# Kernel tuning notes

Measured on AMD Instinct MI355X. Metric: run time of the kernel, lower is better.

## Reference

```python
import jax, jax.numpy as jnp
import numpy as np

B, K, R, H = 64, 256, 4, 32


def setup_inputs() -> dict:
    key = jax.random.key(0)
    ks = jax.random.split(key, 24)
    rn = lambda k, s: jax.random.normal(k, s, dtype=jnp.float32)
    # F.normalize(dim=0) on per-sample [n, R] factors -> normalize columns (axis=1 batched)
    norm_cols = lambda x: x / jnp.linalg.norm(x, axis=1, keepdims=True)
    I = jnp.eye(K, dtype=jnp.float32)
    return dict(
        tensor_input=rn(ks[0], (B, 6, K, K)),
        seed_ic=rn(ks[1], (B, K)),
        seed_sir=rn(ks[2], (B, K)),
        seed_ic_conv=rn(ks[3], (B, K)),
        seed_sir_conv=rn(ks[4], (B, K)),
        scalars=rn(ks[5], (B, 2)),
        second_eig_interlink_out=rn(ks[6], (B,)),
        second_eig_interlink_in=rn(ks[7], (B,)),
        S1=I + 0.1 * rn(ks[8], (K, K)),
        S2=I + 0.1 * rn(ks[9], (K, K)),
        S3=I + 0.1 * rn(ks[10], (K, K)),
        S4=I + 0.1 * rn(ks[11], (K, K)),
        # CP factors (fresh random per sample in torch; fixed here for determinism)
        cp_A=norm_cols(rn(ks[12], (B, 6, R))),
        cp_B=norm_cols(rn(ks[13], (B, K, R))),
        cp_C=norm_cols(rn(ks[14], (B, K, R))),
        cp_W1=0.1 * rn(ks[15], (R, H, 3)), cp_b1=jnp.zeros((R, H), jnp.float32),
        cp_w2=0.1 * rn(ks[16], (R, H)), cp_b2=jnp.zeros((R,), jnp.float32),
        seed_W1=0.1 * rn(ks[17], (4, H, K)), seed_b1=jnp.zeros((4, H), jnp.float32),
        seed_w2=0.1 * rn(ks[18], (4, H)), seed_b2=jnp.zeros((4,), jnp.float32),
        fin_W1=0.1 * rn(ks[19], (H, R + 6)), fin_b1=jnp.zeros((H,), jnp.float32),
        fin_w2=0.1 * rn(ks[20], (H,)), fin_b2=jnp.zeros((), jnp.float32),
    )


def reference(tensor_input, seed_ic, seed_sir, seed_ic_conv, seed_sir_conv, scalars,
              second_eig_interlink_out, second_eig_interlink_in,
              S1, S2, S3, S4, cp_A, cp_B, cp_C,
              cp_W1, cp_b1, cp_w2, cp_b2,
              seed_W1, seed_b1, seed_w2, seed_b2,
              fin_W1, fin_b1, fin_w2, fin_b2):
    Kd = S1.shape[0]
    I = jnp.eye(Kd, dtype=tensor_input.dtype)
    ic1, ic2, sir1, sir2 = tensor_input[:, 0], tensor_input[:, 1], tensor_input[:, 2], tensor_input[:, 3]
    Z1r, Z2r = tensor_input[:, 4], tensor_input[:, 5]

    # MatrixTransform chains == plain batched matmuls (custom backward = standard matmul vjp)
    Z1 = ((ic1 @ S1) @ Z1r @ S2) @ jnp.swapaxes(sir2, -1, -2)   # [B,K,K]
    Z2 = ((sir1 @ S3) @ Z2r @ S4) @ jnp.swapaxes(ic2, -1, -2)   # [B,K,K]

    def spec_loss(val, M):
        ev = jnp.linalg.eigvalsh(M)                 # ascending, lower-triangle (matches torch)
        eig_loss = jnp.mean(jnp.abs(val - ev[1:5])) # k = min(5, K) = 5
        diff = jnp.mean(jnp.abs(M - I))             # reg_loss and diff_from_identity are identical
        off_loss = -jnp.mean(jnp.abs(M - jnp.diag(jnp.diag(M))))
        loss = eig_loss + 0.1 * diff + 0.1 * diff + 0.1 * off_loss
        return jnp.where(val != 0.0, loss, jnp.zeros_like(loss))  # torch: `if value`

    spec_out = jax.vmap(spec_loss)(second_eig_interlink_out, Z1).mean()
    spec_in = jax.vmap(spec_loss)(second_eig_interlink_in, Z2).mean()

    # S-matrix regularizers (batch-independent) + per-sample transform loss.
    # The torch list interleaves them, so the mean = 0.5*s_total + 0.5*mean(transform).
    sreg = lambda S: -jnp.mean(jnp.abs(S - I)) - jnp.mean(jnp.abs(S - jnp.diag(jnp.diag(S))))
    s_total = sreg(S1) + sreg(S2) + sreg(S3) + sreg(S4)
    transform = jnp.mean(jnp.abs(Z1 - Z1r), axis=(1, 2)) + jnp.mean(jnp.abs(Z2 - Z2r), axis=(1, 2))
    s_matrix_mean = 0.5 * s_total + 0.5 * transform.mean()

    # CP reconstruction loss on tensor with slots 4,5 replaced by Z1,Z2
    T_upd = jnp.concatenate([tensor_input[:, :4], Z1[:, None], Z2[:, None]], axis=1)  # [B,6,K,K]
    recon = jnp.einsum('bir,bjr,bkr->bijk', cp_A, cp_B, cp_C)
    cp_loss = jnp.mean((recon - T_upd) ** 2)

    # Per-rank tiny MLPs on factor means
    triple = jnp.stack([cp_A.mean(axis=1), cp_B.mean(axis=1), cp_C.mean(axis=1)], axis=-1)  # [B,R,3]
    h = jax.nn.relu(jnp.einsum('brd,rhd->brh', triple, cp_W1) + cp_b1[None])
    cp_s = jnp.einsum('brh,rh->br', h, cp_w2) + cp_b2[None]                                 # [B,R]

    seeds = jnp.stack([seed_ic, seed_sir, seed_ic_conv, seed_sir_conv], axis=1)             # [B,4,K]
    h2 = jax.nn.relu(jnp.einsum('bjk,jhk->bjh', seeds, seed_W1) + seed_b1[None])
    seed_s = jnp.einsum('bjh,jh->bj', h2, seed_w2) + seed_b2[None]                          # [B,4]

    combined = jnp.concatenate([cp_s, seed_s, scalars], axis=1)                             # [B,R+6]
    logits = jax.nn.relu(combined @ fin_W1.T + fin_b1) @ fin_w2 + fin_b2                    # [B]

    return (logits, spec_out, spec_in, cp_loss, s_matrix_mean)
```

## Files before the change

### kernel.cpp

```cpp
#include <hip/hip_runtime.h>
#include <hip/hip_fp16.h>

#define LM 20

#define OFF_MP    0ull
#define OFF_Q0    16777216ull
#define OFF_Q1    33554432ull
#define OFF_ZB    33554432ull
#define OFF_EIG   50331648ull
#define OFF_DIFFP (OFF_EIG + 4096ull)
#define OFF_OFFP  (OFF_DIFFP + 1024ull)
#define OFF_TRP   (OFF_OFFP + 1024ull)
#define OFF_SMALL (OFF_TRP + 1024ull)

typedef unsigned short ushort_t;
typedef short bf16x8 __attribute__((ext_vector_type(8)));
typedef float f32x4 __attribute__((ext_vector_type(4)));

static __device__ __forceinline__ ushort_t f2bf(float f) {
  unsigned u = __float_as_uint(f);
  unsigned r = (u + 0x7fffu + ((u >> 16) & 1u)) >> 16;
  return (ushort_t)r;
}
static __device__ __forceinline__ unsigned packbf(float a, float b) {
  return (unsigned)f2bf(a) | ((unsigned)f2bf(b) << 16);
}
static __device__ __forceinline__ float bflo(unsigned u) { return __uint_as_float(u << 16); }
static __device__ __forceinline__ float bfhi(unsigned u) { return __uint_as_float(u & 0xffff0000u); }
static __device__ __forceinline__ float b2f(ushort_t u) { return __uint_as_float(((unsigned)u) << 16); }
static __device__ __forceinline__ __half2 u2h2(unsigned u) { __half2 r; *reinterpret_cast<unsigned*>(&r) = u; return r; }
static __device__ __forceinline__ unsigned packh2(float a, float b) {
  return (unsigned)__half_as_ushort(__float2half_rn(a)) |
         ((unsigned)__half_as_ushort(__float2half_rn(b)) << 16);
}

template<bool ABF, int BMODE, bool INITP, bool REDUCE>
__global__ __launch_bounds__(256) void gemm_mfma(
    const void* __restrict__ A0, const void* __restrict__ A1, size_t sA,
    const void* __restrict__ B0, const void* __restrict__ B1, size_t sB,
    void* __restrict__ Cbase, size_t sC,
    const float* __restrict__ Zr0, const float* __restrict__ Zr1, size_t sZr,
    double* __restrict__ smallp, double* __restrict__ diffP,
    double* __restrict__ offP, double* __restrict__ trP)
{
  __shared__ ushort_t At[128][40];
  __shared__ ushort_t Bt[128][40];
  __shared__ float redsh[4][3];
  const int t = threadIdx.x;
  if (INITP && blockIdx.x == 0 && blockIdx.y == 0 && blockIdx.z == 0) {
    if (t < 2) smallp[t] = 0.0;
    if (t < 128) { diffP[t] = 0.0; offP[t] = 0.0; trP[t] = 0.0; }
  }
  const int b = blockIdx.z;
  const int bl = (b < 64) ? b : b - 64;
  const void* Ab_ = (b < 64) ? A0 : A1;
  const void* Bb_ = (b < 64) ? B0 : B1;
  const int tm = blockIdx.y * 128, tn = blockIdx.x * 128;
  const int w = t >> 6, l = t & 63;
  const int wr = w >> 1, wc = w & 1;
  const int fr = l & 15, kc = l >> 4;

  f32x4 acc[4][4] = {};

  for (int s8 = 0; s8 < 8; ++s8) {
    const int k0 = s8 << 5;
    #pragma unroll
    for (int cc = 0; cc < 2; ++cc) {
      int c = t + cc * 256;
      int row = c >> 2, q = c & 3;
      if (ABF) {
        const ushort_t* Ap = (const ushort_t*)Ab_ + (size_t)bl * sA + (size_t)(tm + row) * 256 + k0 + q * 8;
        *(uint4*)&At[row][q * 8] = *(const uint4*)Ap;
      } else {
        const float* Ap = (const float*)Ab_ + (size_t)bl * sA + (size_t)(tm + row) * 256 + k0 + q * 8;
        float4 f0 = *(const float4*)Ap, f1 = *(const float4*)(Ap + 4);
        uint4 u;
        u.x = packbf(f0.x, f0.y); u.y = packbf(f0.z, f0.w);
        u.z = packbf(f1.x, f1.y); u.w = packbf(f1.z, f1.w);
        *(uint4*)&At[row][q * 8] = u;
      }
    }
    if (BMODE == 1) {
      #pragma unroll
      for (int cc = 0; cc < 2; ++cc) {
        int c = t + cc * 256;
        int row = c >> 2, q = c & 3;
        const float* Bp = (const float*)Bb_ + (size_t)bl * sB + (size_t)(tn + row) * 256 + k0 + q * 8;
        float4 f0 = *(const float4*)Bp, f1 = *(const float4*)(Bp + 4);
        uint4 u;
        u.x = packbf(f0.x, f0.y); u.y = packbf(f0.z, f0.w);
        u.z = packbf(f1.x, f1.y); u.w = packbf(f1.z, f1.w);
        *(uint4*)&Bt[row][q * 8] = u;
      }
    } else {
      int k2 = t & 15, c = t >> 4;
      const float* Bp0 = (const float*)Bb_ + (size_t)bl * sB + (size_t)(k0 + 2 * k2) * 256 + tn + c * 8;
      const float* Bp1 = Bp0 + 256;
      float4 a0 = *(const float4*)Bp0, a1 = *(const float4*)(Bp0 + 4);
      float4 c0v = *(const float4*)Bp1, c1v = *(const float4*)(Bp1 + 4);
      float lo[8] = {a0.x,a0.y,a0.z,a0.w,a1.x,a1.y,a1.z,a1.w};
      float hi[8] = {c0v.x,c0v.y,c0v.z,c0v.w,c1v.x,c1v.y,c1v.z,c1v.w};
      unsigned* Bd = (unsigned*)&Bt[0][0];
      #pragma unroll
      for (int i = 0; i < 8; ++i) {
        int n = c * 8 + i;
        Bd[n * 20 + k2] = packbf(lo[i], hi[i]);
      }
    }
    __syncthreads();
    bf16x8 af[4], bfv[4];
    #pragma unroll
    for (int i = 0; i < 4; ++i) af[i] = *(const bf16x8*)&At[wr * 64 + i * 16 + fr][kc * 8];
    #pragma unroll
    for (int jj = 0; jj < 4; ++jj) bfv[jj] = *(const bf16x8*)&Bt[wc * 64 + jj * 16 + fr][kc * 8];
    #pragma unroll
    for (int i = 0; i < 4; ++i) {
      #pragma unroll
      for (int jj = 0; jj < 4; ++jj) {
        acc[i][jj] = __builtin_amdgcn_mfma_f32_16x16x32_bf16(af[i], bfv[jj], acc[i][jj], 0, 0, 0);
      }
    }
    __syncthreads();
  }

  ushort_t* Cp = (ushort_t*)Cbase + (size_t)b * sC;
  #pragma unroll
  for (int i = 0; i < 4; ++i) {
    #pragma unroll
    for (int q = 0; q < 4; ++q) {
      size_t rbase = (size_t)(tm + wr * 64 + i * 16 + kc * 4 + q) * 256;
      #pragma unroll
      for (int jj = 0; jj < 4; ++jj) {
        Cp[rbase + tn + wc * 64 + jj * 16 + fr] = f2bf(acc[i][jj][q]);
      }
    }
  }

  if (REDUCE) {
    const float* Zr_ = ((b < 64) ? Zr0 : Zr1) + (size_t)bl * sZr;
    float pd = 0.f, po = 0.f, ptr = 0.f;
    #pragma unroll
    for (int i = 0; i < 4; ++i) {
      #pragma unroll
      for (int q = 0; q < 4; ++q) {
        int row = tm + wr * 64 + i * 16 + kc * 4 + q;
        const float* ZrRow = Zr_ + (size_t)row * 256 + tn + wc * 64;
        #pragma unroll
        for (int jj = 0; jj < 4; ++jj) {
          int col = tn + wc * 64 + jj * 16 + fr;
          float c = acc[i][jj][q];
          float zr = ZrRow[jj * 16 + fr];
          bool diag = (row == col);
          pd += fabsf(c - (diag ? 1.0f : 0.0f));
          po += diag ? 0.0f : fabsf(c);
          ptr += fabsf(c - zr);
        }
      }
    }
    #pragma unroll
    for (int off = 32; off > 0; off >>= 1) {
      pd += __shfl_down(pd, off);
      po += __shfl_down(po, off);
      ptr += __shfl_down(ptr, off);
    }
    if (l == 0) { redsh[w][0] = pd; redsh[w][1] = po; redsh[w][2] = ptr; }
    __syncthreads();
    if (t == 0) {
      atomicAdd(&diffP[b], (double)(redsh[0][0] + redsh[1][0] + redsh[2][0] + redsh[3][0]));
      atomicAdd(&offP[b],  (double)(redsh[0][1] + redsh[1][1] + redsh[2][1] + redsh[3][1]));
      atomicAdd(&trP[b],   (double)(redsh[0][2] + redsh[1][2] + redsh[2][2] + redsh[3][2]));
    }
  }
}

__global__ __launch_bounds__(256) void symm_t(const ushort_t* __restrict__ Zb,
                                              unsigned* __restrict__ Mp)
{
  __shared__ unsigned Au[64][38];
  __shared__ unsigned Bu[64][38];
  const int blk = blockIdx.x;
  const int mtx = blk / 10, p = blk - mtx * 10;
  const int bi_t[10] = {0,0,0,0,1,1,1,2,2,3};
  const int bj_t[10] = {0,1,2,3,1,2,3,2,3,3};
  const int bi = bi_t[p], bj = bj_t[p];
  const ushort_t* Z = Zb + (size_t)mtx * 65536;
  const int t = threadIdx.x;
  #pragma unroll
  for (int it = 0; it < 4; ++it) {
    int idx = t + it * 256;
    int row = idx >> 4, jj = idx & 15;
    uint2 va = *(const uint2*)(Z + (size_t)(bi * 64 + row) * 256 + bj * 64 + jj * 4);
    uint2 vb = *(const uint2*)(Z + (size_t)(bj * 64 + row) * 256 + bi * 64 + jj * 4);
    Au[row][jj * 2] = va.x; Au[row][jj * 2 + 1] = va.y;
    Bu[row][jj * 2] = vb.x; Bu[row][jj * 2 + 1] = vb.y;
  }
  __syncthreads();
  const float SC = 0.5f * 0.015625f;
  const int r = t & 63, kbase = (t >> 6) * 8;
  unsigned* MpM = Mp + (size_t)mtx * 32768;
  const bool odd = (r & 1);
  #pragma unroll
  for (int i = 0; i < 8; ++i) {
    int k = kbase + i;
    unsigned a = Au[r][k];
    unsigned bu0 = Bu[2 * k][r >> 1], bu1 = Bu[2 * k + 1][r >> 1];
    float b0 = odd ? bfhi(bu0) : bflo(bu0);
    float b1 = odd ? bfhi(bu1) : bflo(bu1);
    MpM[(size_t)(bj * 32 + k) * 256 + bi * 64 + r] =
        packh2((bflo(a) + b0) * SC, (bfhi(a) + b1) * SC);
  }
  if (bi != bj) {
    #pragma unroll
    for (int i = 0; i < 8; ++i) {
      int k = kbase + i;
      unsigned a = Bu[r][k];
      unsigned au0 = Au[2 * k][r >> 1], au1 = Au[2 * k + 1][r >> 1];
      float a0 = odd ? bfhi(au0) : bflo(au0);
      float a1 = odd ? bfhi(au1) : bflo(au1);
      MpM[(size_t)(bi * 32 + k) * 256 + bj * 64 + r] =
          packh2((bflo(a) + a0) * SC, (bfhi(a) + a1) * SC);
    }
  }
}

struct LanSh {
  unsigned vpack[128];
  float wtmp[4][256];
  float red2[4][2];
  float red1[16];
  float alpha[LM];
  float betaArr[LM + 1];
  float beta2arr[LM + 1];
};
struct CpSh { float Bsh[4][256][4]; float Csh[4][256][4]; double red[4][256]; };
struct SregSh { double red[4][256]; };
struct HeadSh {
  float Wl[32][258];
  float seedsl[8][256];
  float hbuf2[8][128];
  float tri[8][4][3];
  float cps[8][4];
  float seds[8][4];
};
union MegaSh { LanSh lan; CpSh cp; SregSh sreg; HeadSh head; };

__global__ __launch_bounds__(1024, 1) void mega_kernel(
    const unsigned* __restrict__ Mp, float* __restrict__ eig,
    const float* __restrict__ ti, const ushort_t* __restrict__ Zb,
    const float* __restrict__ cpA, const float* __restrict__ cpB, const float* __restrict__ cpC,
    double* __restrict__ smallp,
    const float* __restrict__ S1, const float* __restrict__ S2,
    const float* __restrict__ S3, const float* __restrict__ S4,
    const float* __restrict__ seed_ic, const float* __restrict__ seed_sir,
    const float* __restrict__ seed_icc, const float* __restrict__ seed_sirc,
    const float* __restrict__ scalars,
    const float* __restrict__ cpW1, const float* __restrict__ cpb1,
    const float* __restrict__ cpw2, const float* __restrict__ cpb2,
    const float* __restrict__ sW1, const float* __restrict__ sb1,
    const float* __restrict__ sw2, const float* __restrict__ sb2,
    const float* __restrict__ fW1, const float* __restrict__ fb1,
    const float* __restrict__ fw2, const float* __restrict__ fb2,
    float* __restrict__ out)
{
  __shared__ MegaSh sh;
  const int bid = blockIdx.x;
  const int t = threadIdx.x;

  if (bid < 128) {
    int lane = t & 63, w16 = t >> 6;
    int r = t & 255, h = t >> 8;
    int mtx = bid;
    const unsigned* Mb = Mp + (size_t)mtx * 32768 + r;
    unsigned m[32];
    #pragma unroll
    for (int q = 0; q < 32; ++q) m[q] = Mb[(size_t)(h * 32 + q) * 256];

    unsigned u0 = (unsigned)r * 1103515245u + 12345u;
    float r0v = 0.05f + (float)((u0 >> 9) & 0x7FFF) * (1.0f / 32768.0f);
    float vt = 0.0f, vprev = 0.0f;
    {
      float nv = r0v * r0v;
      #pragma unroll
      for (int off = 32; off > 0; off >>= 1) nv += __shfl_down(nv, off);
      if (lane == 0) sh.lan.red1[w16] = nv;
    }
    __syncthreads();
    {
      float nrm2 = sh.lan.red1[0] + sh.lan.red1[1] + sh.lan.red1[2] + sh.lan.red1[3];
      vt = r0v * rsqrtf(nrm2);
      if (h == 0) {
        float vo = __shfl_down(vt, 1);
        if ((lane & 1) == 0) sh.lan.vpack[t >> 1] = packh2(vt, vo);
      }
    }
    __syncthreads();

    const uint4* vp4 = (const uint4*)sh.lan.vpack;
    float2* red2 = (float2*)&sh.lan.red2[0][0];
    float beta_prev = 0.0f;
    int meff = LM;
    for (int j = 0; j < LM; ++j) {
      __half2 h0v = u2h2(0u), h1v = u2h2(0u), h2v = u2h2(0u), h3v = u2h2(0u);
      #pragma unroll
      for (int q = 0; q < 8; ++q) {
        uint4 vu = vp4[h * 8 + q];
        h0v = __hfma2(u2h2(m[4 * q + 0]), u2h2(vu.x), h0v);
        h1v = __hfma2(u2h2(m[4 * q + 1]), u2h2(vu.y), h1v);
        h2v = __hfma2(u2h2(m[4 * q + 2]), u2h2(vu.z), h2v);
        h3v = __hfma2(u2h2(m[4 * q + 3]), u2h2(vu.w), h3v);
      }
      float2 f0 = __half22float2(h0v), f1 = __half22float2(h1v);
      float2 f2 = __half22float2(h2v), f3 = __half22float2(h3v);
      sh.lan.wtmp[h][r] = ((f0.x + f0.y) + (f1.x + f1.y)) + ((f2.x + f2.y) + (f3.x + f3.y));
      float wt = 0.0f;
      __syncthreads();
      if (h == 0) {
        wt = sh.lan.wtmp[0][r] + sh.lan.wtmp[1][r] + sh.lan.wtmp[2][r] + sh.lan.wtmp[3][r];
        float s1 = wt * vt, s3 = wt * wt;
        #pragma unroll
        for (int off = 32; off > 0; off >>= 1) {
          s1 += __shfl_down(s1, off);
          s3 += __shfl_down(s3, off);
        }
        if (lane == 0) red2[w16] = make_float2(s1, s3);
      }
      __syncthreads();
      float2 p0 = red2[0], p1 = red2[1], p2 = red2[2], p3 = red2[3];
      float S1v = ((p0.x + p1.x) + (p2.x + p3.x));
      float S3v = ((p0.y + p1.y) + (p2.y + p3.y));
      float bn2 = S3v - S1v * S1v - beta_prev * beta_prev;
      float bn = sqrtf(fmaxf(bn2, 1e-30f));
      if (t == 0) { sh.lan.alpha[j] = S1v; sh.lan.betaArr[j + 1] = bn; sh.lan.beta2arr[j + 1] = bn * bn; }
      if (bn < 1e-6f * (fabsf(S1v) + 1.0f)) { meff = j + 1; break; }
      if (h == 0) {
        float wn = (wt - S1v * vt - beta_prev * vprev) / bn;
        vprev = vt; vt = wn;
        float vo = __shfl_down(vt, 1);
        if ((lane & 1) == 0) sh.lan.vpack[t >> 1] = packh2(vt, vo);
      }
      beta_prev = bn;
      __syncthreads();
    }
    __syncthreads();

    if (w16 < 4) {
      float lo = 1e30f, hi = -1e30f;
      for (int i = 0; i < meff; ++i) {
        float bl = (i > 0) ? sh.lan.betaArr[i] : 0.0f;
        float bu = (i + 1 < meff) ? sh.lan.betaArr[i + 1] : 0.0f;
        lo = fminf(lo, sh.lan.alpha[i] - bl - bu);
        hi = fmaxf(hi, sh.lan.alpha[i] + bl + bu);
      }
      int q = w16 + 1; if (q > meff - 1) q = meff - 1;
      #pragma unroll
      for (int rr = 0; rr < 3; ++rr) {
        float step = (hi - lo) * (1.0f / 65.0f);
        float mid = lo + step * (float)(lane + 1);
        int cnt = 0;
        float d = sh.lan.alpha[0] - mid;
        if (fabsf(d) < 1e-20f) d = -1e-20f;
        cnt += (d < 0.0f);
        for (int i = 1; i < meff; ++i) {
          d = sh.lan.alpha[i] - mid - sh.lan.beta2arr[i] / d;
          if (fabsf(d) < 1e-20f) d = -1e-20f;
          cnt += (d < 0.0f);
        }
        unsigned long long mask = __ballot(cnt >= q + 1);
        if (mask == 0ULL) {
          lo = lo + step * 64.0f;
        } else {
          int idx = __ffsll(mask) - 1;
          float nlo = lo + step * (float)idx;
          hi = lo + step * (float)(idx + 1);
          lo = nlo;
        }
      }
      if (lane == 0) eig[mtx * 4 + w16] = 32.0f * (lo + hi);
    }
  } else if (bid < 244) {
    int g = t >> 8, tid = t & 255;
    int unit = (bid - 128) * 4 + g;
    bool live = (unit < 384);
    int b = live ? (unit / 6) : 0;
    int i = live ? (unit - b * 6) : 0;
    float (*Bsh)[4] = sh.cp.Bsh[g];
    float (*Csh)[4] = sh.cp.Csh[g];
    double* red = sh.cp.red[g];
    if (live) {
      *(float4*)&Bsh[tid][0] = *(const float4*)(cpB + ((size_t)b * 256 + tid) * 4);
      *(float4*)&Csh[tid][0] = *(const float4*)(cpC + ((size_t)b * 256 + tid) * 4);
    }
    float a0 = live ? cpA[((size_t)b * 6 + i) * 4 + 0] : 0.f;
    float a1 = live ? cpA[((size_t)b * 6 + i) * 4 + 1] : 0.f;
    float a2 = live ? cpA[((size_t)b * 6 + i) * 4 + 2] : 0.f;
    float a3 = live ? cpA[((size_t)b * 6 + i) * 4 + 3] : 0.f;
    __syncthreads();
    double acc0 = 0, acc1 = 0;
    if (live) {
      float c0 = Csh[tid][0], c1 = Csh[tid][1], c2 = Csh[tid][2], c3 = Csh[tid][3];
      if (i < 4) {
        const float* T = ti + ((size_t)b * 6 + i) * 65536;
        #pragma unroll 4
        for (int j = 0; j < 256; j += 2) {
          float4 bj0 = *(const float4*)&Bsh[j][0];
          float4 bj1 = *(const float4*)&Bsh[j + 1][0];
          float r0 = a0 * bj0.x * c0 + a1 * bj0.y * c1 + a2 * bj0.z * c2 + a3 * bj0.w * c3;
          float r1 = a0 * bj1.x * c0 + a1 * bj1.y * c1 + a2 * bj1.z * c2 + a3 * bj1.w * c3;
          float d0 = r0 - T[(size_t)j * 256 + tid];
          float d1 = r1 - T[(size_t)(j + 1) * 256 + tid];
          acc0 += (double)d0 * (double)d0;
          acc1 += (double)d1 * (double)d1;
        }
      } else {
        const ushort_t* T = Zb + (size_t)((i == 4) ? b : 64 + b) * 65536;
        #pragma unroll 4
        for (int j = 0; j < 256; j += 2) {
          float4 bj0 = *(const float4*)&Bsh[j][0];
          float4 bj1 = *(const float4*)&Bsh[j + 1][0];
          float r0 = a0 * bj0.x * c0 + a1 * bj0.y * c1 + a2 * bj0.z * c2 + a3 * bj0.w * c3;
          float r1 = a0 * bj1.x * c0 + a1 * bj1.y * c1 + a2 * bj1.z * c2 + a3 * bj1.w * c3;
          float d0 = r0 - b2f(T[(size_t)j * 256 + tid]);
          float d1 = r1 - b2f(T[(size_t)(j + 1) * 256 + tid]);
          acc0 += (double)d0 * (double)d0;
          acc1 += (double)d1 * (double)d1;
        }
      }
    }
    red[tid] = acc0 + acc1; __syncthreads();
    #pragma unroll
    for (int s = 128; s > 0; s >>= 1) { if (tid < s) red[tid] += red[tid + s]; __syncthreads(); }
    if (live && tid == 0) atomicAdd(&smallp[0], red[0]);
  } else if (bid < 248) {
    int g = t >> 8, tid = t & 255;
    int slot = (bid - 244) * 4 + g;
    int mnum = slot >> 2, quarter = slot & 3;
    const float* S = (mnum == 0) ? S1 : (mnum == 1) ? S2 : (mnum == 2) ? S3 : S4;
    double* red = sh.sreg.red[g];
    double tot = 0;
    int base = quarter * 16384;
    #pragma unroll 4
    for (int e = base + tid; e < base + 16384; e += 256) {
      int i = e >> 8, j = e & 255;
      float a = S[e];
      tot += (double)fabsf(a - (i == j ? 1.0f : 0.0f));
      if (i != j) tot += (double)fabsf(a);
    }
    red[tid] = tot; __syncthreads();
    #pragma unroll
    for (int s = 128; s > 0; s >>= 1) { if (tid < s) red[tid] += red[tid + s]; __syncthreads(); }
    if (tid == 0) atomicAdd(&smallp[1], -red[0] / 65536.0);
  } else {
    HeadSh& H = sh.head;
    const int b0 = (bid - 248) * 8;
    const int g = t >> 6, l = t & 63;
    const bool act = g < 8;
    const int b = b0 + (act ? g : 0);
    if (act) {
      if (l < 4) {
        float s = 0;
        #pragma unroll
        for (int i = 0; i < 6; ++i) s += cpA[((size_t)b * 6 + i) * 4 + l];
        H.tri[g][l][0] = s * (1.0f / 6.0f);
      }
      float4 sB = make_float4(0,0,0,0), sC = make_float4(0,0,0,0);
      for (int j = l; j < 256; j += 64) {
        float4 v = *(const float4*)(cpB + ((size_t)b * 256 + j) * 4);
        sB.x += v.x; sB.y += v.y; sB.z += v.z; sB.w += v.w;
        float4 w = *(const float4*)(cpC + ((size_t)b * 256 + j) * 4);
        sC.x += w.x; sC.y += w.y; sC.z += w.z; sC.w += w.w;
      }
      #pragma unroll
      for (int off = 32; off > 0; off >>= 1) {
        sB.x += __shfl_down(sB.x, off); sB.y += __shfl_down(sB.y, off);
        sB.z += __shfl_down(sB.z, off); sB.w += __shfl_down(sB.w, off);
        sC.x += __shfl_down(sC.x, off); sC.y += __shfl_down(sC.y, off);
        sC.z += __shfl_down(sC.z, off); sC.w += __shfl_down(sC.w, off);
      }
      if (l == 0) {
        H.tri[g][0][1] = sB.x * (1.0f/256.0f); H.tri[g][1][1] = sB.y * (1.0f/256.0f);
        H.tri[g][2][1] = sB.z * (1.0f/256.0f); H.tri[g][3][1] = sB.w * (1.0f/256.0f);
        H.tri[g][0][2] = sC.x * (1.0f/256.0f); H.tri[g][1][2] = sC.y * (1.0f/256.0f);
        H.tri[g][2][2] = sC.z * (1.0f/256.0f); H.tri[g][3][2] = sC.w * (1.0f/256.0f);
      }
      if (l < 4) {
        float s = 0;
        for (int hh = 0; hh < 32; ++hh) {
          float z = cpb1[l * 32 + hh];
          #pragma unroll
          for (int d = 0; d < 3; ++d) z += H.tri[g][l][d] * cpW1[(l * 32 + hh) * 3 + d];
          z = fmaxf(z, 0.0f);
          s += z * cpw2[l * 32 + hh];
        }
        H.cps[g][l] = s + cpb2[l];
      }
    }
    #pragma unroll 1
    for (int j = 0; j < 4; ++j) {
      __syncthreads();
      for (int idx = t; idx < 8192; idx += 1024) {
        H.Wl[idx >> 8][idx & 255] = sW1[(size_t)(j * 32 + (idx >> 8)) * 256 + (idx & 255)];
      }
      const float* sarr = (j == 0) ? seed_ic : (j == 1) ? seed_sir : (j == 2) ? seed_icc : seed_sirc;
      for (int idx = t; idx < 2048; idx += 1024) {
        H.seedsl[idx >> 8][idx & 255] = sarr[(size_t)(b0 + (idx >> 8)) * 256 + (idx & 255)];
      }
      __syncthreads();
      int bb = t >> 7, o = (t >> 2) & 31, kq = t & 3;
      float d = 0.f;
      #pragma unroll
      for (int kk = 0; kk < 64; kk += 4) {
        float4 w = *(const float4*)&H.Wl[o][kq * 64 + kk];
        float4 s = *(const float4*)&H.seedsl[bb][kq * 64 + kk];
        d += w.x * s.x + w.y * s.y + w.z * s.z + w.w * s.w;
      }
      d += __shfl_xor(d, 1);
      d += __shfl_xor(d, 2);
      if (kq == 0) {
        float z = fmaxf(d + sb1[j * 32 + o], 0.0f);
        H.hbuf2[bb][j * 32 + o] = z * sw2[j * 32 + o];
      }
    }
    __syncthreads();
    if (act && l < 4) {
      float s = 0;
      #pragma unroll
      for (int hh = 0; hh < 32; ++hh) s += H.hbuf2[g][l * 32 + hh];
      H.seds[g][l] = s + sb2[l];
    }
    __syncthreads();
    float av2 = 0.0f;
    if (act && l < 32) {
      float z = fb1[l];
      #pragma unroll
      for (int d = 0; d < 10; ++d) {
        float cd = (d < 4) ? H.cps[g][d] : (d < 8) ? H.seds[g][d - 4] : scalars[b * 2 + (d - 8)];
        z += cd * fW1[l * 10 + d];
      }
      z = fmaxf(z, 0.0f);
      av2 = z * fw2[l];
    }
    #pragma unroll
    for (int off = 16; off > 0; off >>= 1) av2 += __shfl_down(av2, off);
    if (act && l == 0) out[b] = av2 + fb2[0];
  }
}

__global__ __launch_bounds__(64) void combine_kernel(const float* __restrict__ eig,
    const double* __restrict__ diffP, const double* __restrict__ offP, const double* __restrict__ trP,
    const float* __restrict__ valo, const float* __restrict__ vali,
    const double* __restrict__ smallp, float* __restrict__ out)
{
  int l = threadIdx.x;
  float vo = valo[l], vi = vali[l];
  float el = 0, el2 = 0;
  #pragma unroll
  for (int e = 0; e < 4; ++e) {
    el  += fabsf(vo - eig[l * 4 + e]);
    el2 += fabsf(vi - eig[(64 + l) * 4 + e]);
  }
  float lo_ = el * 0.25f + 0.2f * (float)(diffP[l] * (1.0/65536.0)) - 0.1f * (float)(offP[l] * (1.0/65536.0));
  float li_ = el2 * 0.25f + 0.2f * (float)(diffP[64 + l] * (1.0/65536.0)) - 0.1f * (float)(offP[64 + l] * (1.0/65536.0));
  if (vo == 0.0f) lo_ = 0.0f;
  if (vi == 0.0f) li_ = 0.0f;
  float trb = (float)((trP[l] + trP[64 + l]) * (1.0/65536.0));
  #pragma unroll
  for (int off = 32; off > 0; off >>= 1) {
    lo_ += __shfl_down(lo_, off);
    li_ += __shfl_down(li_, off);
    trb += __shfl_down(trb, off);
  }
  if (l == 0) {
    out[64] = lo_ * (1.0f / 64.0f);
    out[65] = li_ * (1.0f / 64.0f);
    out[66] = (float)(smallp[0] / (64.0 * 6.0 * 65536.0));
    out[67] = 0.5f * (float)smallp[1] + 0.5f * (trb * (1.0f / 64.0f));
  }
}

extern "C" void kernel_launch(void* const* d_in, const int* in_sizes, int n_in,
                              void* d_out, int out_size, void* d_ws, size_t ws_size,
                              hipStream_t stream) {
  (void)in_sizes; (void)n_in; (void)out_size; (void)ws_size;
  const float* ti       = (const float*)d_in[0];
  const float* seed_ic  = (const float*)d_in[1];
  const float* seed_sir = (const float*)d_in[2];
  const float* seed_icc = (const float*)d_in[3];
  const float* seed_sirc= (const float*)d_in[4];
  const float* scalars  = (const float*)d_in[5];
  const float* valo     = (const float*)d_in[6];
  const float* vali     = (const float*)d_in[7];
  const float* S1p      = (const float*)d_in[8];
  const float* S2p      = (const float*)d_in[9];
  const float* S3p      = (const float*)d_in[10];
  const float* S4p      = (const float*)d_in[11];
  const float* cpA      = (const float*)d_in[12];
  const float* cpB      = (const float*)d_in[13];
  const float* cpC      = (const float*)d_in[14];
  const float* cpW1     = (const float*)d_in[15];
  const float* cpb1     = (const float*)d_in[16];
  const float* cpw2     = (const float*)d_in[17];
  const float* cpb2     = (const float*)d_in[18];
  const float* sW1      = (const float*)d_in[19];
  const float* sb1      = (const float*)d_in[20];
  const float* sw2      = (const float*)d_in[21];
  const float* sb2      = (const float*)d_in[22];
  const float* fW1      = (const float*)d_in[23];
  const float* fb1      = (const float*)d_in[24];
  const float* fw2      = (const float*)d_in[25];
  const float* fb2      = (const float*)d_in[26];

  char* ws = (char*)d_ws;
  unsigned* Mp     = (unsigned*)(ws + OFF_MP);
  ushort_t* Q0     = (ushort_t*)(ws + OFF_Q0);
  ushort_t* Q1     = (ushort_t*)(ws + OFF_Q1);
  ushort_t* Zb     = (ushort_t*)(ws + OFF_ZB);
  float*    eig    = (float*)(ws + OFF_EIG);
  double*   diffP  = (double*)(ws + OFF_DIFFP);
  double*   offP   = (double*)(ws + OFF_OFFP);
  double*   trP    = (double*)(ws + OFF_TRP);
  double*   smallp = (double*)(ws + OFF_SMALL);
  float*    out    = (float*)d_out;

  dim3 gg(2, 2, 128), gb(256);
  const size_t S6 = 6ull * 65536ull, S1b = 65536ull;
  gemm_mfma<false, 2, true, false><<<gg, gb, 0, stream>>>(
      (const void*)(ti + 0 * 65536), (const void*)(ti + 2 * 65536), S6,
      (const void*)S1p, (const void*)S3p, 0,
      (void*)Q0, S1b, nullptr, nullptr, 0, smallp, diffP, offP, trP);
  gemm_mfma<true, 2, false, false><<<gg, gb, 0, stream>>>(
      (const void*)Q0, (const void*)(Q0 + 64 * 65536), S1b,
      (const void*)(ti + 4 * 65536), (const void*)(ti + 5 * 65536), S6,
      (void*)Q1, S1b, nullptr, nullptr, 0, smallp, diffP, offP, trP);
  gemm_mfma<true, 2, false, false><<<gg, gb, 0, stream>>>(
      (const void*)Q1, (const void*)(Q1 + 64 * 65536), S1b,
      (const void*)S2p, (const void*)S4p, 0,
      (void*)Q0, S1b, nullptr, nullptr, 0, smallp, diffP, offP, trP);
  gemm_mfma<true, 1, false, true><<<gg, gb, 0, stream>>>(
      (const void*)Q0, (const void*)(Q0 + 64 * 65536), S1b,
      (const void*)(ti + 3 * 65536), (const void*)(ti + 1 * 65536), S6,
      (void*)Zb, S1b,
      ti + 4 * 65536, ti + 5 * 65536, S6, smallp, diffP, offP, trP);

  symm_t<<<1280, 256, 0, stream>>>(Zb, Mp);

  mega_kernel<<<256, 1024, 0, stream>>>(
      Mp, eig, ti, Zb, cpA, cpB, cpC, smallp,
      S1p, S2p, S3p, S4p,
      seed_ic, seed_sir, seed_icc, seed_sirc, scalars,
      cpW1, cpb1, cpw2, cpb2, sW1, sb1, sw2, sb2,
      fW1, fb1, fw2, fb2, out);

  combine_kernel<<<1, 64, 0, stream>>>(eig, diffP, offP, trP, valo, vali, smallp, out);
}
```

Baseline: 137.9 us.

## Fuse symmetrization transpose into mega kernel via shared-memory Z tile

Removes the separate symm_t kernel that built the symmetrized, scaled half-precision matrix in global memory. Each Lanczos block in mega_kernel now loads its whole 256x256 bf16 Z matrix into a padded shared-memory buffer and builds its register-resident M entries from Z and its transpose on the fly. This drops one kernel launch and a global write/read round trip. In exchange the LanSh union grows by about 130 KB of LDS, and the column reads of the transpose may hit bank conflicts.

```diff
diff --git a/kernel.cpp b/kernel.cpp
--- a/kernel.cpp
+++ b/kernel.cpp
@@ -3,7 +3,6 @@
 
 #define LM 20
 
-#define OFF_MP    0ull
 #define OFF_Q0    16777216ull
 #define OFF_Q1    33554432ull
 #define OFF_ZB    33554432ull
@@ -173,57 +172,8 @@
   }
 }
 
-__global__ __launch_bounds__(256) void symm_t(const ushort_t* __restrict__ Zb,
-                                              unsigned* __restrict__ Mp)
-{
-  __shared__ unsigned Au[64][38];
-  __shared__ unsigned Bu[64][38];
-  const int blk = blockIdx.x;
-  const int mtx = blk / 10, p = blk - mtx * 10;
-  const int bi_t[10] = {0,0,0,0,1,1,1,2,2,3};
-  const int bj_t[10] = {0,1,2,3,1,2,3,2,3,3};
-  const int bi = bi_t[p], bj = bj_t[p];
-  const ushort_t* Z = Zb + (size_t)mtx * 65536;
-  const int t = threadIdx.x;
-  #pragma unroll
-  for (int it = 0; it < 4; ++it) {
-    int idx = t + it * 256;
-    int row = idx >> 4, jj = idx & 15;
-    uint2 va = *(const uint2*)(Z + (size_t)(bi * 64 + row) * 256 + bj * 64 + jj * 4);
-    uint2 vb = *(const uint2*)(Z + (size_t)(bj * 64 + row) * 256 + bi * 64 + jj * 4);
-    Au[row][jj * 2] = va.x; Au[row][jj * 2 + 1] = va.y;
-    Bu[row][jj * 2] = vb.x; Bu[row][jj * 2 + 1] = vb.y;
-  }
-  __syncthreads();
-  const float SC = 0.5f * 0.015625f;
-  const int r = t & 63, kbase = (t >> 6) * 8;
-  unsigned* MpM = Mp + (size_t)mtx * 32768;
-  const bool odd = (r & 1);
-  #pragma unroll
-  for (int i = 0; i < 8; ++i) {
-    int k = kbase + i;
-    unsigned a = Au[r][k];
-    unsigned bu0 = Bu[2 * k][r >> 1], bu1 = Bu[2 * k + 1][r >> 1];
-    float b0 = odd ? bfhi(bu0) : bflo(bu0);
-    float b1 = odd ? bfhi(bu1) : bflo(bu1);
-    MpM[(size_t)(bj * 32 + k) * 256 + bi * 64 + r] =
-        packh2((bflo(a) + b0) * SC, (bfhi(a) + b1) * SC);
-  }
-  if (bi != bj) {
-    #pragma unroll
-    for (int i = 0; i < 8; ++i) {
-      int k = kbase + i;
-      unsigned a = Bu[r][k];
-      unsigned au0 = Au[2 * k][r >> 1], au1 = Au[2 * k + 1][r >> 1];
-      float a0 = odd ? bfhi(au0) : bflo(au0);
-      float a1 = odd ? bfhi(au1) : bflo(au1);
-      MpM[(size_t)(bi * 32 + k) * 256 + bj * 64 + r] =
-          packh2((bflo(a) + a0) * SC, (bfhi(a) + a1) * SC);
-    }
-  }
-}
-
 struct LanSh {
+  ushort_t Zl[256][260];
   unsigned vpack[128];
   float wtmp[4][256];
   float red2[4][2];
@@ -245,7 +195,7 @@
 union MegaSh { LanSh lan; CpSh cp; SregSh sreg; HeadSh head; };
 
 __global__ __launch_bounds__(1024, 1) void mega_kernel(
-    const unsigned* __restrict__ Mp, float* __restrict__ eig,
+    float* __restrict__ eig,
     const float* __restrict__ ti, const ushort_t* __restrict__ Zb,
     const float* __restrict__ cpA, const float* __restrict__ cpB, const float* __restrict__ cpC,
     double* __restrict__ smallp,
@@ -270,10 +220,27 @@
     int lane = t & 63, w16 = t >> 6;
     int r = t & 255, h = t >> 8;
     int mtx = bid;
-    const unsigned* Mb = Mp + (size_t)mtx * 32768 + r;
+    const ushort_t* Zm = Zb + (size_t)mtx * 65536;
+
+    #pragma unroll
+    for (int it = 0; it < 16; ++it) {
+      int idx = t + it * 1024;
+      int row = idx >> 6, c4 = (idx & 63) << 2;
+      *(uint2*)&sh.lan.Zl[row][c4] = *(const uint2*)(Zm + (size_t)row * 256 + c4);
+    }
+    __syncthreads();
+
+    const float SC = 0.5f * 0.015625f;
     unsigned m[32];
     #pragma unroll
-    for (int q = 0; q < 32; ++q) m[q] = Mb[(size_t)(h * 32 + q) * 256];
+    for (int q = 0; q < 32; ++q) {
+      int c0 = h * 64 + 2 * q;
+      unsigned a = *(const unsigned*)&sh.lan.Zl[r][c0];
+      float b0v = b2f(sh.lan.Zl[c0][r]);
+      float b1v = b2f(sh.lan.Zl[c0 + 1][r]);
+      m[q] = packh2((bflo(a) + b0v) * SC, (bfhi(a) + b1v) * SC);
+    }
+    __syncthreads();
 
     unsigned u0 = (unsigned)r * 1103515245u + 12345u;
     float r0v = 0.05f + (float)((u0 >> 9) & 0x7FFF) * (1.0f / 32768.0f);
@@ -610,7 +577,6 @@
   const float* fb2      = (const float*)d_in[26];
 
   char* ws = (char*)d_ws;
-  unsigned* Mp     = (unsigned*)(ws + OFF_MP);
   ushort_t* Q0     = (ushort_t*)(ws + OFF_Q0);
   ushort_t* Q1     = (ushort_t*)(ws + OFF_Q1);
   ushort_t* Zb     = (ushort_t*)(ws + OFF_ZB);
@@ -641,10 +607,8 @@
       (void*)Zb, S1b,
       ti + 4 * 65536, ti + 5 * 65536, S6, smallp, diffP, offP, trP);
 
-  symm_t<<<1280, 256, 0, stream>>>(Zb, Mp);
-
   mega_kernel<<<256, 1024, 0, stream>>>(
-      Mp, eig, ti, Zb, cpA, cpB, cpC, smallp,
+      eig, ti, Zb, cpA, cpB, cpC, smallp,
       S1p, S2p, S3p, S4p,
       seed_ic, seed_sir, seed_icc, seed_sirc, scalars,
       cpW1, cpb1, cpw2, cpb2, sW1, sb1, sw2, sb2,
```

Measured after the change: 130.9 us, median of 2. -5.1%, faster.
